# Performance work log

Hardware: AMD Instinct MI355X
Metric: run time of the kernel (lower is better)

## Reference

```python
import jax, jax.numpy as jnp
import numpy as np

B = 4096          # trees (characters)
T = 16            # nodes per tree template
VC, VO = 2000, 16
D, H = 256, 512


def _build_trees(rng):
    # template: perfect binary tree depth 3 (nodes 0..14, leaves 7..14) + extra leaf 15
    # node 3 is ternary with third child 15
    left_t = np.full(T, -1, np.int32)
    right_t = np.full(T, -1, np.int32)
    third_t = np.full(T, -1, np.int32)
    for i in range(7):
        left_t[i] = 2 * i + 1
        right_t[i] = 2 * i + 2
    third_t[3] = 15
    off = (np.arange(B, dtype=np.int32) * T)[:, None]
    def shift(t):
        return np.where(t[None, :] >= 0, t[None, :] + off, -1).ravel().astype(np.int32)
    left, right, third = shift(left_t), shift(right_t), shift(third_t)
    comp = np.zeros((B, T), np.int32)
    comp[:, 7:] = rng.integers(1, VC, size=(B, 9))      # leaves get real components
    op = np.zeros((B, T), np.int32)
    op[:, :7] = rng.integers(1, VO, size=(B, 7))        # internal nodes get operators
    lvl0 = (off + np.array([0])).ravel().astype(np.int32)
    lvl1 = (off + np.array([1, 2])).ravel().astype(np.int32)
    lvl2 = (off + np.array([3, 4, 5, 6])).ravel().astype(np.int32)
    return comp.ravel(), op.ravel(), left, right, third, lvl2, lvl1, lvl0


def setup_inputs() -> dict:
    rng = np.random.default_rng(0)
    comp, op, left, right, third, lvl2, lvl1, lvl0 = _build_trees(rng)
    def xavier(fi, fo):
        s = np.sqrt(6.0 / (fi + fo))
        return jnp.asarray(rng.uniform(-s, s, size=(fi, fo)).astype(np.float32))
    comp_table = rng.normal(0, 0.02, size=(VC, D)).astype(np.float32)
    comp_table[0] = 0.0  # padding_idx
    op_table = rng.normal(0, 0.02, size=(VO, D)).astype(np.float32)
    op_table[0] = 0.0
    return {
        'component_ids': jnp.asarray(comp), 'operator_ids': jnp.asarray(op),
        'left_child': jnp.asarray(left), 'right_child': jnp.asarray(right),
        'third_child': jnp.asarray(third),
        'lvl2_idx': jnp.asarray(lvl2), 'lvl1_idx': jnp.asarray(lvl1), 'lvl0_idx': jnp.asarray(lvl0),
        'comp_table': jnp.asarray(comp_table), 'op_table': jnp.asarray(op_table),
        'W1b': xavier(3 * D, H), 'b1b': jnp.zeros((H,), jnp.float32),
        'W2b': xavier(H, D), 'b2b': jnp.zeros((D,), jnp.float32),
        'W1t': xavier(4 * D, H), 'b1t': jnp.zeros((H,), jnp.float32),
        'W2t': xavier(H, D), 'b2t': jnp.zeros((D,), jnp.float32),
        'gamma': jnp.ones((D,), jnp.float32), 'beta': jnp.zeros((D,), jnp.float32),
    }


def _ln(x, gamma, beta, eps=1e-5):
    mu = jnp.mean(x, axis=-1, keepdims=True)
    var = jnp.mean(jnp.square(x - mu), axis=-1, keepdims=True)
    return (x - mu) * jax.lax.rsqrt(var + eps) * gamma + beta


def reference(component_ids, operator_ids, left_child, right_child, third_child,
              lvl2_idx, lvl1_idx, lvl0_idx,
              comp_table, op_table, W1b, b1b, W2b, b2b, W1t, b1t, W2t, b2t,
              gamma, beta):
    node_embeds = comp_table[component_ids]               # [N, D]
    for idx in (lvl2_idx, lvl1_idx, lvl0_idx):            # bottom-up levels
        op_e = op_table[operator_ids[idx]]                # [L, D]
        le = node_embeds[left_child[idx]]
        re = node_embeds[right_child[idx]]
        ti = third_child[idx]
        has3 = (ti >= 0)
        te = node_embeds[jnp.maximum(ti, 0)] * has3[:, None].astype(node_embeds.dtype)
        b_in = jnp.concatenate([op_e, le, re], axis=-1)   # [L, 3D]
        b_out = jax.nn.gelu(b_in @ W1b + b1b, approximate=False) @ W2b + b2b
        t_in = jnp.concatenate([op_e, le, re, te], axis=-1)  # [L, 4D]
        t_out = jax.nn.gelu(t_in @ W1t + b1t, approximate=False) @ W2t + b2t
        new_b = _ln(b_out + le + re, gamma, beta)
        new_t = _ln(t_out + (le + re + te) / 3.0, gamma, beta)
        new = jnp.where(has3[:, None], new_t, new_b)
        node_embeds = node_embeds.at[idx].set(new)
    return node_embeds[lvl0_idx]                          # [B, D] root embeddings (eval: no dropout)
```

## Files before the change

### kernel.cpp

```cpp
#include <hip/hip_runtime.h>

typedef __bf16 bf16_t;
typedef __attribute__((ext_vector_type(8))) __bf16 bf16x8;
typedef __attribute__((ext_vector_type(4))) __bf16 bf16x4;
typedef __attribute__((ext_vector_type(4))) float f32x4;

#define GLL16(gsrc, ldst) __builtin_amdgcn_global_load_lds( \
    (const __attribute__((address_space(1))) void*)(gsrc),  \
    (__attribute__((address_space(3))) void*)(ldst), 16, 0, 0)
#define SBAR() __builtin_amdgcn_s_barrier()
#define SCHED0() __builtin_amdgcn_sched_barrier(0)

__global__ void prep(const void* __restrict__ op_table, bf16_t* __restrict__ opb,
                     const void* __restrict__ comp_table, bf16_t* __restrict__ ctb,
                     const void* __restrict__ W1b, bf16_t* __restrict__ W1bp,
                     const void* __restrict__ W1t, bf16_t* __restrict__ W1tp,
                     const void* __restrict__ W2b, bf16_t* __restrict__ W2bp,
                     const void* __restrict__ W2t, bf16_t* __restrict__ W2tp,
                     int* __restrict__ flag,
                     const int* __restrict__ lvl2, const int* __restrict__ lvl1,
                     const int* __restrict__ lvl0, const int* __restrict__ third,
                     int* __restrict__ lists, int* __restrict__ cnts,
                     int* __restrict__ inv) {
    int b = blockIdx.x, tid = threadIdx.x;
    if (b >= 828) {
        int r = (b - 828) * 256 + tid;
        int slot, lr, base_t, base_b;
        const int* lvl;
        if (r < 16384)      { slot = 0; lr = r;         lvl = lvl2; base_t = 0;     base_b = 16384; }
        else if (r < 24576) { slot = 1; lr = r - 16384; lvl = lvl1; base_t = 32768; base_b = 40960; }
        else                { slot = 2; lr = r - 24576; lvl = lvl0; base_t = 49152; base_b = 53248; }
        int node = lvl[lr];
        int tern = third[node] >= 0 ? 1 : 0;
        if (slot == 0)      inv[node] = lr;
        else if (slot == 1) inv[node] = 16384 + lr;

        unsigned long long bt = __ballot(tern);
        unsigned long long bb = __ballot(!tern);
        int lane = tid & 63;
        unsigned long long ltm = (1ull << lane) - 1ull;
        int post = __popcll(bt & ltm), posb = __popcll(bb & ltm);
        int baseT = 0, baseB = 0;
        if (lane == 0) {
            baseT = atomicAdd(&cnts[slot * 2 + 1], __popcll(bt));
            baseB = atomicAdd(&cnts[slot * 2 + 0], __popcll(bb));
        }
        baseT = __shfl(baseT, 0, 64);
        baseB = __shfl(baseB, 0, 64);
        lists[tern ? (base_t + baseT + post) : (base_b + baseB + posb)] = lr;
        return;
    }
    int isbf;
    {
        const unsigned short* cts = (const unsigned short*)comp_table;
        int ok = 1;
        for (int i = 0; i < 16; i++) {
            int e = (cts[256 + i] >> 7) & 0xFF;
            ok &= (e >= 80 && e <= 126) ? 1 : 0;
        }
        isbf = ok;
    }
    if (b == 0 && tid == 0) *flag = isbf;

    if (b < 252) {
        int i0 = (b < 2) ? (b * 256 + tid) * 8 : ((b - 2) * 256 + tid) * 8;
        const void* s = (b < 2) ? op_table : comp_table;
        bf16_t* d = (b < 2) ? opb : ctb;
        if (isbf) {
            *(bf16x8*)(d + i0) = *(const bf16x8*)((const bf16_t*)s + i0);
        } else {
            const float* fp = (const float*)s + i0;
            bf16_t tmp[8];
            for (int z = 0; z < 8; z++) tmp[z] = (bf16_t)fp[z];
            *(bf16x8*)(d + i0) = *(bf16x8*)tmp;
        }
        return;
    }
    const void* src; bf16_t* dst; int c0_, Nshift;
    if (b < 444)      { src = W1b; dst = W1bp; c0_ = (b - 252) * 256; Nshift = 9; }
    else if (b < 700) { src = W1t; dst = W1tp; c0_ = (b - 444) * 256; Nshift = 9; }
    else if (b < 764) { src = W2b; dst = W2bp; c0_ = (b - 700) * 256; Nshift = 8; }
    else              { src = W2t; dst = W2tp; c0_ = (b - 764) * 256; Nshift = 8; }
    const int N = 1 << Nshift;
    int idx = c0_ + tid;
    int kc  = idx >> (Nshift + 2);
    int rem = idx & ((N << 2) - 1);
    int gp  = rem >> Nshift;
    int n   = rem & (N - 1);
    int g_log = gp ^ ((n >> 1) & 3);
    int kbase = kc * 32 + g_log * 8;
    bf16_t tmp[8];
    if (isbf) {
        const bf16_t* sp = (const bf16_t*)src;
        for (int i = 0; i < 8; i++) tmp[i] = sp[((size_t)(kbase + i) << Nshift) + n];
    } else {
        const float* sp = (const float*)src;
        for (int i = 0; i < 8; i++) tmp[i] = (bf16_t)sp[((size_t)(kbase + i) << Nshift) + n];
    }
    *(bf16x8*)(dst + (size_t)(((kc << Nshift) + n) << 5) + (gp << 3)) = *(bf16x8*)tmp;
}

__device__ __forceinline__ void load8f(const bf16_t* ne2, const void* ct, int isbf,
                                       int invn, int cidn, int q, float* o) {
    if (invn >= 0) {
        bf16x8 v = *(const bf16x8*)(ne2 + (size_t)invn * 256 + q);
        for (int z = 0; z < 8; z++) o[z] = (float)v[z];
    } else if (isbf) {
        bf16x8 v = *(const bf16x8*)((const bf16_t*)ct + (size_t)cidn * 256 + q);
        for (int z = 0; z < 8; z++) o[z] = (float)v[z];
    } else {
        const float* fp = (const float*)ct + (size_t)cidn * 256 + q;
        f32x4 a = *(const f32x4*)fp, b = *(const f32x4*)(fp + 4);
        for (int z = 0; z < 4; z++) { o[z] = a[z]; o[z + 4] = b[z]; }
    }
}

__device__ __forceinline__ float ldparam(const void* p, int i, int isbf) {
    return isbf ? (float)((const bf16_t*)p)[i] : ((const float*)p)[i];
}

__global__ __launch_bounds__(512, 2) void fused_level(
    const int* __restrict__ list_t, const int* __restrict__ list_b,
    const int* __restrict__ cntpair, const int* __restrict__ lvl_idx,
    const int* __restrict__ op_ids, const int* __restrict__ lch,
    const int* __restrict__ rch, const int* __restrict__ tch,
    bf16_t* __restrict__ ne2, const bf16_t* __restrict__ opb,
    const void* __restrict__ ct, const bf16_t* __restrict__ ctb,
    const int* __restrict__ cid, const int* __restrict__ inv,
    const int* __restrict__ flagp,
    const bf16_t* __restrict__ W1tp, const void* __restrict__ b1t,
    const bf16_t* __restrict__ W2tp, const void* __restrict__ b2t,
    const bf16_t* __restrict__ W1bp, const void* __restrict__ b1b,
    const bf16_t* __restrict__ W2bp, const void* __restrict__ b2b,
    const void* __restrict__ gma, const void* __restrict__ bta,
    int slotBase, void* __restrict__ out)
{
    __shared__ __align__(1024) char smem[81920];

    const int tid = threadIdx.x;
    const int w = tid >> 6, lane = tid & 63, cc = lane & 15, qq = lane >> 4;
    const int gx = (cc >> 1) & 3;
    const int e7 = cc & 7;
    const int cnt_t = cntpair[1], cnt_b = cntpair[0];
    const int blocks_t = (cnt_t + 63) >> 6;
    int tern, base, cnt, K1c;
    const int* list;
    const bf16_t *W1p, *W2p;
    const void *b1, *b2;
    if ((int)blockIdx.x < blocks_t) {
        tern = 1; list = list_t; base = blockIdx.x * 64; cnt = cnt_t;
        W1p = W1tp; b1 = b1t; W2p = W2tp; b2 = b2t; K1c = 32;
    } else {
        tern = 0; list = list_b; base = (blockIdx.x - blocks_t) * 64; cnt = cnt_b;
        if (base >= cnt) return;
        W1p = W1bp; b1 = b1b; W2p = W2bp; b2 = b2b; K1c = 24;
    }
    const int act = min(64, cnt - base);
    const int isbf = *flagp;

    int glA = 0, opSA = 0;
    int aInv0 = 0, aInv1 = 0, aInv2 = 0, aCid0 = 0, aCid1 = 0, aCid2 = 0;
    if (tid < 256) {
        int rowA = tid >> 2;
        glA = (tid & 3) ^ ((rowA >> 1) & 3);
        int rA = list[base + min(rowA, act - 1)];
        int nA = lvl_idx[rA];
        opSA = op_ids[nA];
        int a0 = lch[nA], a1 = rch[nA];
        int a2 = tern ? tch[nA] : a0;
        aInv0 = inv[a0]; aInv1 = inv[a1]; aInv2 = inv[a2];
        aCid0 = aInv0 < 0 ? cid[a0] : 0;
        aCid1 = aInv1 < 0 ? cid[a1] : 0;
        aCid2 = aInv2 < 0 ? cid[a2] : 0;
    }

    const int ms = tid >> 3, gs = tid & 7;
    const int lr = list[base + min(ms, act - 1)];
    const int node = lvl_idx[lr];
    const int c0 = lch[node], c1 = rch[node];
    const int c2 = tern ? tch[node] : c0;
    int sInv[3] = {inv[c0], inv[c1], inv[c2]};
    int sCid[3];
    sCid[0] = sInv[0] < 0 ? cid[c0] : 0;
    sCid[1] = sInv[1] < 0 ? cid[c1] : 0;
    sCid[2] = sInv[2] < 0 ? cid[c2] : 0;

    float b2f[2], gf[2], btf[2];
    for (int j = 0; j < 2; j++) {
        int col = (w + 8 * j) * 16 + cc;
        b2f[j] = ldparam(b2, col, isbf);
        gf[j] = ldparam(gma, col, isbf);
        btf[j] = ldparam(bta, col, isbf);
    }

    const f32x4 zf = {0.f, 0.f, 0.f, 0.f};
    f32x4 acc1[4][4];
    for (int m = 0; m < 4; m++) for (int j = 0; j < 4; j++) acc1[m][j] = zf;

#define STAGE1(kc_, bsel_) do {                                                   \
        const char* srcb_ = (const char*)W1p + ((size_t)(kc_) << 15);             \
        char* dstb_ = smem + ((bsel_) << 15);                                     \
        _Pragma("unroll")                                                         \
        for (int i_ = 0; i_ < 4; i_++) {                                          \
            int off_ = ((i_ << 3) + w) << 10;                                     \
            GLL16(srcb_ + off_ + (lane << 4), dstb_ + off_);                      \
        }                                                                         \
        if (w < 4) {                                                              \
            int colg_ = (kc_) * 32 + glA * 8;                                     \
            int piece_ = colg_ >> 8, po_ = colg_ & 255;                           \
            int iv_ = piece_ == 1 ? aInv0 : piece_ == 2 ? aInv1 : aInv2;          \
            int cd_ = piece_ == 1 ? aCid0 : piece_ == 2 ? aCid1 : aCid2;          \
            const bf16_t* s_ = piece_ == 0 ? opb + (size_t)opSA * 256             \
                : (iv_ >= 0 ? ne2 + (size_t)iv_ * 256 : ctb + (size_t)cd_ * 256); \
            GLL16(s_ + po_, smem + 65536 + ((bsel_) << 12) + (w << 10));          \
        }                                                                         \
    } while (0)

    STAGE1(0, 0);
    for (int kc = 0; kc < K1c; kc++) {
        const int cur = kc & 1;
        const bool more = kc + 1 < K1c;
        if (more) STAGE1(kc + 1, cur ^ 1);
        if (more) {
            if (w < 4) asm volatile("s_waitcnt vmcnt(5)" ::: "memory");
            else       asm volatile("s_waitcnt vmcnt(4)" ::: "memory");
        } else {
            asm volatile("s_waitcnt vmcnt(0)" ::: "memory");
        }
        SCHED0();
        SBAR();
        SCHED0();
        const bf16_t* as = (const bf16_t*)(smem + 65536 + (cur << 12));
        const bf16_t* bs = (const bf16_t*)(smem + (cur << 15));
        bf16x8 af[4];
        for (int m = 0; m < 4; m++)
            af[m] = *(const bf16x8*)(as + (m * 16 + cc) * 32 + ((qq ^ gx) << 3));
        __builtin_amdgcn_s_setprio(1);
        for (int j = 0; j < 4; j++) {
            bf16x8 bv = *(const bf16x8*)(bs + ((w + 8 * j) * 16 + cc) * 32 + ((qq ^ gx) << 3));
            for (int m = 0; m < 4; m++)
                acc1[m][j] = __builtin_amdgcn_mfma_f32_16x16x32_bf16(bv, af[m], acc1[m][j], 0, 0, 0);
        }
        __builtin_amdgcn_s_setprio(0);
        SCHED0();
        SBAR();
    }

#define STAGE2(kc_) do {                                                          \
        const char* srcb_ = (const char*)W2p + ((size_t)(kc_) << 14);             \
        _Pragma("unroll")                                                         \
        for (int i_ = 0; i_ < 2; i_++) {                                          \
            int off_ = ((i_ << 3) + w) << 10;                                     \
            GLL16(srcb_ + off_ + (lane << 4), smem + off_);                       \
        }                                                                         \
    } while (0)

    STAGE2(0);
    {
        unsigned short* Hs = (unsigned short*)(smem + 16384);
        for (int j = 0; j < 4; j++) {
            float b1q[4];
            for (int r = 0; r < 4; r++) b1q[r] = ldparam(b1, (w + 8 * j) * 16 + qq * 4 + r, isbf);
            int c16 = ((w + 8 * j) << 1) + (qq >> 1);
            for (int m = 0; m < 4; m++) {
                int row = m * 16 + cc;
                bf16x4 hv;
                for (int r = 0; r < 4; r++) {
                    float v = acc1[m][j][r] + b1q[r];
                    hv[r] = (bf16_t)(0.5f * v * (1.0f + erff(v * 0.70710678118654752f)));
                }
                *(bf16x4*)(Hs + (row << 9) + ((c16 ^ e7) << 3) + ((qq & 1) << 2)) = hv;
            }
        }
    }
    asm volatile("s_waitcnt vmcnt(0) lgkmcnt(0)" ::: "memory");
    SCHED0();
    SBAR();
    SCHED0();

    f32x4 acc2[4][2];
    for (int m = 0; m < 4; m++) for (int j = 0; j < 2; j++) acc2[m][j] = zf;
    for (int kc = 0; kc < 16; kc++) {
        const unsigned short* Hs = (const unsigned short*)(smem + 16384);
        const bf16_t* bs = (const bf16_t*)smem;
        bf16x8 af[4];
        for (int m = 0; m < 4; m++)
            af[m] = *(const bf16x8*)(Hs + ((m * 16 + cc) << 9) + ((((kc << 2) + qq) ^ e7) << 3));
        __builtin_amdgcn_s_setprio(1);
        for (int j = 0; j < 2; j++) {
            bf16x8 bv = *(const bf16x8*)(bs + ((w + 8 * j) * 16 + cc) * 32 + ((qq ^ gx) << 3));
            for (int m = 0; m < 4; m++)
                acc2[m][j] = __builtin_amdgcn_mfma_f32_16x16x32_bf16(af[m], bv, acc2[m][j], 0, 0, 0);
        }
        __builtin_amdgcn_s_setprio(0);
        SCHED0();
        SBAR();
        SCHED0();
        if (kc + 1 < 16) {
            STAGE2(kc + 1);
            asm volatile("s_waitcnt vmcnt(0)" ::: "memory");
            SCHED0();
            SBAR();
            SCHED0();
        }
    }
    __syncthreads();

    {
        float* Rf = (float*)(smem + 16384);
        int colb = gs * 32;
        for (int i = 0; i < 4; i++) {
            int q = colb + i * 8;
            float lv[8], rv[8], tv[8];
            load8f(ne2, ct, isbf, sInv[0], sCid[0], q, lv);
            load8f(ne2, ct, isbf, sInv[1], sCid[1], q, rv);
            if (tern) load8f(ne2, ct, isbf, sInv[2], sCid[2], q, tv);
            f32x4 s0, s1;
            if (tern) {
                for (int z = 0; z < 4; z++) {
                    s0[z] = (lv[z] + rv[z] + tv[z]) * (1.0f / 3.0f);
                    s1[z] = (lv[z + 4] + rv[z + 4] + tv[z + 4]) * (1.0f / 3.0f);
                }
            } else {
                for (int z = 0; z < 4; z++) {
                    s0[z] = lv[z] + rv[z];
                    s1[z] = lv[z + 4] + rv[z + 4];
                }
            }
            *(f32x4*)(Rf + ms * 256 + q) = s0;
            *(f32x4*)(Rf + ms * 256 + q + 4) = s1;
        }
    }
    __syncthreads();

    float* partS = (float*)smem;
    float* partQ = partS + 512;
    float* muA   = partQ + 512;
    float* rsA   = muA + 64;
    const float* Rf = (const float*)(smem + 16384);

    for (int m = 0; m < 4; m++) for (int r = 0; r < 4; r++) {
        int row = m * 16 + qq * 4 + r;
        float ps = 0.f, pq = 0.f;
        for (int j = 0; j < 2; j++) {
            int col = (w + 8 * j) * 16 + cc;
            float x = acc2[m][j][r] + b2f[j] + Rf[(row << 8) + col];
            acc2[m][j][r] = x;
            ps += x; pq += x * x;
        }
        for (int d = 1; d < 16; d <<= 1) {
            ps += __shfl_xor(ps, d, 64);
            pq += __shfl_xor(pq, d, 64);
        }
        if (cc == 0) { partS[w * 64 + row] = ps; partQ[w * 64 + row] = pq; }
    }
    __syncthreads();
    if (tid < 64) {
        float s = 0.f, sq = 0.f;
        for (int i = 0; i < 8; i++) {
            s  += partS[i * 64 + tid];
            sq += partQ[i * 64 + tid];
        }
        float mu = s * (1.0f / 256.0f);
        float var = sq * (1.0f / 256.0f) - mu * mu;
        muA[tid] = mu;
        rsA[tid] = rsqrtf(fmaxf(var, 0.0f) + 1e-5f);
    }
    __syncthreads();

    for (int m = 0; m < 4; m++) for (int r = 0; r < 4; r++) {
        int row = m * 16 + qq * 4 + r;
        if (row >= act) continue;
        float mu = muA[row], rs = rsA[row];
        int lr2 = list[base + row];
        for (int j = 0; j < 2; j++) {
            int col = (w + 8 * j) * 16 + cc;
            float y = (acc2[m][j][r] - mu) * rs * gf[j] + btf[j];
            if (out) {
                if (isbf) ((bf16_t*)out)[(size_t)lr2 * 256 + col] = (bf16_t)y;
                else      ((float*)out)[(size_t)lr2 * 256 + col] = y;
            } else {
                ne2[(size_t)(slotBase + lr2) * 256 + col] = (bf16_t)y;
            }
        }
    }
#undef STAGE1
#undef STAGE2
}

extern "C" void kernel_launch(void* const* d_in, const int* in_sizes, int n_in,
                              void* d_out, int out_size, void* d_ws, size_t ws_size,
                              hipStream_t stream) {
    const int* cid    = (const int*)d_in[0];
    const int* opids  = (const int*)d_in[1];
    const int* lch    = (const int*)d_in[2];
    const int* rch    = (const int*)d_in[3];
    const int* tch    = (const int*)d_in[4];
    const int* lvl2   = (const int*)d_in[5];
    const int* lvl1   = (const int*)d_in[6];
    const int* lvl0   = (const int*)d_in[7];
    const void* comp_table = d_in[8];
    const void* op_table   = d_in[9];
    const void* W1b = d_in[10];
    const void* b1b = d_in[11];
    const void* W2b = d_in[12];
    const void* b2b = d_in[13];
    const void* W1t = d_in[14];
    const void* b1t = d_in[15];
    const void* W2t = d_in[16];
    const void* b2t = d_in[17];
    const void* gma = d_in[18];
    const void* bta = d_in[19];

    char* wsp = (char*)d_ws;
    bf16_t* ne2  = (bf16_t*)wsp;                 size_t off = 12582912;
    bf16_t* opb  = (bf16_t*)(wsp + off);         off += 8192;
    bf16_t* ctb  = (bf16_t*)(wsp + off);         off += 1024000;
    bf16_t* W1bp = (bf16_t*)(wsp + off);         off += 786432;
    bf16_t* W1tp = (bf16_t*)(wsp + off);         off += 1048576;
    bf16_t* W2bp = (bf16_t*)(wsp + off);         off += 262144;
    bf16_t* W2tp = (bf16_t*)(wsp + off);         off += 262144;
    int* inv   = (int*)(wsp + off);              off += 262144;
    int* lists = (int*)(wsp + off);              off += 229376;
    int* cnts  = (int*)(wsp + off);              off += 64;
    int* flag  = cnts + 8;

    hipMemsetAsync(cnts, 0, 64, stream);
    hipMemsetAsync(inv, 0xFF, 262144, stream);
    prep<<<940, 256, 0, stream>>>(op_table, opb, comp_table, ctb,
                                  W1b, W1bp, W1t, W1tp, W2b, W2bp, W2t, W2tp, flag,
                                  lvl2, lvl1, lvl0, tch, lists, cnts, inv);

    fused_level<<<257, 512, 0, stream>>>(lists + 0, lists + 16384, cnts + 0, lvl2,
        opids, lch, rch, tch, ne2, opb, comp_table, ctb, cid, inv, flag,
        W1tp, b1t, W2tp, b2t, W1bp, b1b, W2bp, b2b, gma, bta, 0, nullptr);
    fused_level<<<129, 512, 0, stream>>>(lists + 32768, lists + 40960, cnts + 2, lvl1,
        opids, lch, rch, tch, ne2, opb, comp_table, ctb, cid, inv, flag,
        W1tp, b1t, W2tp, b2t, W1bp, b1b, W2bp, b2b, gma, bta, 16384, nullptr);
    fused_level<<<65, 512, 0, stream>>>(lists + 49152, lists + 53248, cnts + 4, lvl0,
        opids, lch, rch, tch, ne2, opb, comp_table, ctb, cid, inv, flag,
        W1tp, b1t, W2tp, b2t, W1bp, b1b, W2bp, b2b, gma, bta, 0, d_out);
}
```

Measured before the change: 260.9 us.

## Double-buffer W2 tiles and split GELU hidden write into two halves

```diff
diff --git a/kernel.cpp b/kernel.cpp
--- a/kernel.cpp
+++ b/kernel.cpp
@@ -135,7 +135,7 @@
     const void* __restrict__ gma, const void* __restrict__ bta,
     int slotBase, void* __restrict__ out)
 {
-    __shared__ __align__(1024) char smem[81920];
+    __shared__ __align__(1024) char smem[73728];
 
     const int tid = threadIdx.x;
     const int w = tid >> 6, lane = tid & 63, cc = lane & 15, qq = lane >> 4;
@@ -246,46 +246,57 @@
         SBAR();
     }
 
-#define STAGE2(kc_) do {                                                          \
+#define STAGE2(kc_, bsel_) do {                                                   \
         const char* srcb_ = (const char*)W2p + ((size_t)(kc_) << 14);             \
+        char* dstb_ = smem + ((bsel_) << 14);                                     \
         _Pragma("unroll")                                                         \
         for (int i_ = 0; i_ < 2; i_++) {                                          \
             int off_ = ((i_ << 3) + w) << 10;                                     \
-            GLL16(srcb_ + off_ + (lane << 4), smem + off_);                       \
+            GLL16(srcb_ + off_ + (lane << 4), dstb_ + off_);                      \
         }                                                                         \
     } while (0)
-
-    STAGE2(0);
-    {
-        unsigned short* Hs = (unsigned short*)(smem + 16384);
-        for (int j = 0; j < 4; j++) {
-            float b1q[4];
-            for (int r = 0; r < 4; r++) b1q[r] = ldparam(b1, (w + 8 * j) * 16 + qq * 4 + r, isbf);
-            int c16 = ((w + 8 * j) << 1) + (qq >> 1);
-            for (int m = 0; m < 4; m++) {
-                int row = m * 16 + cc;
-                bf16x4 hv;
-                for (int r = 0; r < 4; r++) {
-                    float v = acc1[m][j][r] + b1q[r];
-                    hv[r] = (bf16_t)(0.5f * v * (1.0f + erff(v * 0.70710678118654752f)));
-                }
-                *(bf16x4*)(Hs + (row << 9) + ((c16 ^ e7) << 3) + ((qq & 1) << 2)) = hv;
-            }
-        }
-    }
+#define HWRITE(jb_) do {                                                          \
+        unsigned short* Hs_ = (unsigned short*)(smem + 32768);                    \
+        for (int j_ = (jb_); j_ < (jb_) + 2; j_++) {                              \
+            float b1q_[4];                                                        \
+            for (int r_ = 0; r_ < 4; r_++)                                        \
+                b1q_[r_] = ldparam(b1, (w + 8 * j_) * 16 + qq * 4 + r_, isbf);    \
+            int c16_ = ((w + 8 * (j_ - (jb_))) << 1) + (qq >> 1);                 \
+            for (int m_ = 0; m_ < 4; m_++) {                                      \
+                int row_ = m_ * 16 + cc;                                          \
+                bf16x4 hv_;                                                       \
+                for (int r_ = 0; r_ < 4; r_++) {                                  \
+                    float v_ = acc1[m_][j_][r_] + b1q_[r_];                       \
+                    hv_[r_] = (bf16_t)(0.5f * v_ *                                \
+                        (1.0f + erff(v_ * 0.70710678118654752f)));                \
+                }                                                                 \
+                *(bf16x4*)(Hs_ + (row_ << 8) + (((c16_ ^ e7)) << 3)               \
+                           + ((qq & 1) << 2)) = hv_;                              \
+            }                                                                     \
+        }                                                                         \
+    } while (0)
+
+    f32x4 acc2[4][2];
+    for (int m = 0; m < 4; m++) for (int j = 0; j < 2; j++) acc2[m][j] = zf;
+
+    STAGE2(0, 0);
+    HWRITE(0);
     asm volatile("s_waitcnt vmcnt(0) lgkmcnt(0)" ::: "memory");
     SCHED0();
     SBAR();
     SCHED0();
-
-    f32x4 acc2[4][2];
-    for (int m = 0; m < 4; m++) for (int j = 0; j < 2; j++) acc2[m][j] = zf;
-    for (int kc = 0; kc < 16; kc++) {
-        const unsigned short* Hs = (const unsigned short*)(smem + 16384);
-        const bf16_t* bs = (const bf16_t*)smem;
+    for (int kc = 0; kc < 8; kc++) {
+        const int cur = kc & 1;
+        STAGE2(kc + 1, cur ^ 1);
+        asm volatile("s_waitcnt vmcnt(2)" ::: "memory");
+        SCHED0();
+        SBAR();
+        SCHED0();
+        const unsigned short* Hs = (const unsigned short*)(smem + 32768);
+        const bf16_t* bs = (const bf16_t*)(smem + (cur << 14));
         bf16x8 af[4];
         for (int m = 0; m < 4; m++)
-            af[m] = *(const bf16x8*)(Hs + ((m * 16 + cc) << 9) + ((((kc << 2) + qq) ^ e7) << 3));
+            af[m] = *(const bf16x8*)(Hs + ((m * 16 + cc) << 8) + ((((kc << 2) + qq) ^ e7) << 3));
         __builtin_amdgcn_s_setprio(1);
         for (int j = 0; j < 2; j++) {
             bf16x8 bv = *(const bf16x8*)(bs + ((w + 8 * j) * 16 + cc) * 32 + ((qq ^ gx) << 3));
@@ -295,19 +306,40 @@
         __builtin_amdgcn_s_setprio(0);
         SCHED0();
         SBAR();
-        SCHED0();
-        if (kc + 1 < 16) {
-            STAGE2(kc + 1);
-            asm volatile("s_waitcnt vmcnt(0)" ::: "memory");
-            SCHED0();
-            SBAR();
-            SCHED0();
-        }
+    }
+    HWRITE(2);
+    asm volatile("s_waitcnt lgkmcnt(0)" ::: "memory");
+    SCHED0();
+    SBAR();
+    SCHED0();
+    for (int kc = 8; kc < 16; kc++) {
+        const int cur = kc & 1;
+        const bool more = kc + 1 < 16;
+        if (more) STAGE2(kc + 1, cur ^ 1);
+        if (more) asm volatile("s_waitcnt vmcnt(2)" ::: "memory");
+        else      asm volatile("s_waitcnt vmcnt(0)" ::: "memory");
+        SCHED0();
+        SBAR();
+        SCHED0();
+        const unsigned short* Hs = (const unsigned short*)(smem + 32768);
+        const bf16_t* bs = (const bf16_t*)(smem + (cur << 14));
+        bf16x8 af[4];
+        for (int m = 0; m < 4; m++)
+            af[m] = *(const bf16x8*)(Hs + ((m * 16 + cc) << 8) + (((((kc - 8) << 2) + qq) ^ e7) << 3));
+        __builtin_amdgcn_s_setprio(1);
+        for (int j = 0; j < 2; j++) {
+            bf16x8 bv = *(const bf16x8*)(bs + ((w + 8 * j) * 16 + cc) * 32 + ((qq ^ gx) << 3));
+            for (int m = 0; m < 4; m++)
+                acc2[m][j] = __builtin_amdgcn_mfma_f32_16x16x32_bf16(af[m], bv, acc2[m][j], 0, 0, 0);
+        }
+        __builtin_amdgcn_s_setprio(0);
+        SCHED0();
+        SBAR();
     }
     __syncthreads();
 
     {
-        float* Rf = (float*)(smem + 16384);
+        float* Rf = (float*)smem;
         int colb = gs * 32;
         for (int i = 0; i < 4; i++) {
             int q = colb + i * 8;
@@ -333,11 +365,11 @@
     }
     __syncthreads();
 
-    float* partS = (float*)smem;
+    float* partS = (float*)(smem + 65536);
     float* partQ = partS + 512;
     float* muA   = partQ + 512;
     float* rsA   = muA + 64;
-    const float* Rf = (const float*)(smem + 16384);
+    const float* Rf = (const float*)smem;
 
     for (int m = 0; m < 4; m++) for (int r = 0; r < 4; r++) {
         int row = m * 16 + qq * 4 + r;
@@ -386,6 +418,7 @@
     }
 #undef STAGE1
 #undef STAGE2
+#undef HWRITE
 }
 
 extern "C" void kernel_launch(void* const* d_in, const int* in_sizes, int n_in,
```

New measurement: 248.9 us. -4.6%, faster.
